# Kernel tuning notes

Measured on AMD Instinct MI355X. Metric: run time of the kernel, lower is better.

## Reference

```python
import jax, jax.numpy as jnp
import numpy as np

D_MODEL = 1024
N_HEADS = 16
D_HEAD = 64
B, S = 8, 1024
EPS = 1.1920929e-07  # torch.finfo(float32).eps, RMSNorm default eps=None


def setup_inputs() -> dict:
    key = jax.random.key(0)
    k1, k2, k3 = jax.random.split(key, 3)
    x = jax.random.normal(k1, (B, S, D_MODEL), dtype=jnp.float32)
    W_qkv = jax.random.normal(k2, (3 * N_HEADS * D_HEAD, D_MODEL), dtype=jnp.float32) * 0.02
    b_qkv = jnp.zeros((3 * N_HEADS * D_HEAD,), dtype=jnp.float32)
    W_o = jax.random.normal(k3, (D_MODEL, N_HEADS * D_HEAD), dtype=jnp.float32) * 0.02
    b_o = jnp.zeros((D_MODEL,), dtype=jnp.float32)
    return {"x": x, "W_qkv": W_qkv, "b_qkv": b_qkv, "W_o": W_o, "b_o": b_o}


def reference(x, W_qkv, b_qkv, W_o, b_o):
    # RMSNorm, no affine
    normed = x * jax.lax.rsqrt(jnp.mean(x * x, axis=-1, keepdims=True) + EPS)
    qkv = normed @ W_qkv.T + b_qkv                       # [b, s, 3*H*Dh]
    # packing order '(n_heads d_head n_qkv)' -> reshape (H, Dh, 3), unbind last
    qkv = qkv.reshape(*qkv.shape[:-1], N_HEADS, D_HEAD, 3)
    q, k, v = qkv[..., 0], qkv[..., 1], qkv[..., 2]       # [b, s, H, Dh]
    scores = jnp.einsum('bqhd,bkhd->bhqk', q, k)          # no 1/sqrt(d) scaling
    seq = x.shape[-2]
    causal_mask = jnp.triu(jnp.ones((seq, seq), dtype=bool), k=1)  # True above diag
    scores = jnp.where(causal_mask, -jnp.inf, scores)
    # NOTE: softmax over the QUERY axis (dim=-2), faithful to the source
    attn = jax.nn.softmax(scores, axis=-2)                # [b, h, q, k]
    z = jnp.einsum('bhqk,bkhd->bqhd', attn, v)            # [b, q, H, Dh]
    z = z.reshape(*z.shape[:-2], N_HEADS * D_HEAD)
    return z @ W_o.T + b_o
```

## Files before the change

### kernel.cpp

```cpp
#include <hip/hip_runtime.h>
#include <hip/hip_bf16.h>

typedef _Float16 f16;
typedef _Float16 f16x8 __attribute__((ext_vector_type(8)));
typedef _Float16 f16x4 __attribute__((ext_vector_type(4)));
typedef float f32x4 __attribute__((ext_vector_type(4)));

constexpr int Bb = 8, Ss = 1024, Hh = 16, DH = 64, DM = 1024, N3 = 3072;
constexpr int Mm = Bb * Ss;
constexpr float EPS = 1.1920929e-07f;

__device__ __forceinline__ void gll16(const f16* g, f16* l) {
    __builtin_amdgcn_global_load_lds(
        (__attribute__((address_space(1))) void*)(g),
        (__attribute__((address_space(3))) void*)(l), 16, 0, 0);
}

__global__ void prep_kernel(const float* __restrict__ x, f16* __restrict__ xh,
                            const float* __restrict__ Wqkv, const float* __restrict__ Wo,
                            f16* __restrict__ wq, f16* __restrict__ wo) {
    const int t = threadIdx.x;
    if (blockIdx.x < Mm) {
        const int row = blockIdx.x;
        float4 v = *(const float4*)(x + (size_t)row * DM + t * 4);
        float s = v.x * v.x + v.y * v.y + v.z * v.z + v.w * v.w;
#pragma unroll
        for (int o = 32; o > 0; o >>= 1) s += __shfl_down(s, o, 64);
        __shared__ float red[4];
        if ((t & 63) == 0) red[t >> 6] = s;
        __syncthreads();
        float tot = red[0] + red[1] + red[2] + red[3];
        float sc = rsqrtf(tot * (1.0f / DM) + EPS);
        f16x4 hv = {(f16)(v.x * sc), (f16)(v.y * sc), (f16)(v.z * sc), (f16)(v.w * sc)};
        *(f16x4*)(xh + (size_t)row * DM + t * 4) = hv;
    } else {
        int i = (blockIdx.x - Mm) * 256 + t;
        const int n1 = (N3 * DM) / 4;
        if (i < n1) {
            float4 v = ((const float4*)Wqkv)[i];
            f16x4 h = {(f16)v.x, (f16)v.y, (f16)v.z, (f16)v.w};
            ((f16x4*)wq)[i] = h;
        } else {
            int j = i - n1;
            float4 v = ((const float4*)Wo)[j];
            f16x4 h = {(f16)v.x, (f16)v.y, (f16)v.z, (f16)v.w};
            ((f16x4*)wo)[j] = h;
        }
    }
}

__launch_bounds__(256, 2)
__global__ void qkv_gemm(const f16* __restrict__ xh, const f16* __restrict__ wq,
                         const float* __restrict__ bqkv, f16* __restrict__ qk,
                         f16* __restrict__ vT) {
    __shared__ __align__(16) f16 As[128 * 64];
    __shared__ __align__(16) f16 Bs[128 * 64];
    const int t = threadIdx.x, lane = t & 63, w = t >> 6;
    const int bid = blockIdx.y * gridDim.x + blockIdx.x;
    const int swz = (bid & 7) * 192 + (bid >> 3);
    const int gm0 = (swz / 24) * 128, gn0 = (swz % 24) * 128;
    const int wm = (w >> 1) * 64, wn = (w & 1) * 64;
    const int srow = lane >> 3, sslot = (lane & 7) ^ srow;
    const int r15 = lane & 15, cs = lane >> 4;

    const f16* Ag = xh + (size_t)(gm0 + srow) * DM + sslot * 8;
    const f16* Bg = wq + (size_t)(gn0 + srow) * DM + sslot * 8;

    int aoff[4][2], boff[4][2];
#pragma unroll
    for (int i = 0; i < 4; ++i) {
        int Ra = wm + i * 16 + r15;
        aoff[i][0] = Ra * 64 + ((cs ^ (Ra & 7)) * 8);
        aoff[i][1] = Ra * 64 + (((cs + 4) ^ (Ra & 7)) * 8);
        int Rb = wn + i * 16 + r15;
        boff[i][0] = Rb * 64 + ((cs ^ (Rb & 7)) * 8);
        boff[i][1] = Rb * 64 + (((cs + 4) ^ (Rb & 7)) * 8);
    }
    f32x4 acc[4][4] = {};

    for (int k0 = 0; k0 < DM; k0 += 64) {
        __syncthreads();
#pragma unroll
        for (int j = 0; j < 4; ++j) {
            int c = w * 4 + j;
            gll16(Ag + (size_t)c * 8 * DM + k0, As + c * 512);
            gll16(Bg + (size_t)c * 8 * DM + k0, Bs + c * 512);
        }
        __syncthreads();
#pragma unroll
        for (int half = 0; half < 2; ++half) {
            f16x8 af[4], bf[4];
#pragma unroll
            for (int i = 0; i < 4; ++i) af[i] = *(const f16x8*)&As[aoff[i][half]];
#pragma unroll
            for (int i = 0; i < 4; ++i) bf[i] = *(const f16x8*)&Bs[boff[i][half]];
#pragma unroll
            for (int mi = 0; mi < 4; ++mi)
#pragma unroll
                for (int ni = 0; ni < 4; ++ni)
                    acc[mi][ni] = __builtin_amdgcn_mfma_f32_16x16x32_f16(af[mi], bf[ni], acc[mi][ni], 0, 0, 0);
        }
    }
#pragma unroll
    for (int mi = 0; mi < 4; ++mi) {
#pragma unroll
        for (int ni = 0; ni < 4; ++ni) {
            int jcol = gn0 + wn + ni * 16 + r15;
            float bb = bqkv[jcol];
            int h = jcol / 192, r = jcol % 192;
            int d = r / 3, which = r % 3;
            int m0 = gm0 + wm + mi * 16 + cs * 4;
            int b = m0 >> 10, s0 = m0 & 1023;
            int bh = b * Hh + h;
            if (which == 2) {
                f16x4 pv = {(f16)(acc[mi][ni][0] + bb), (f16)(acc[mi][ni][1] + bb),
                            (f16)(acc[mi][ni][2] + bb), (f16)(acc[mi][ni][3] + bb)};
                *(f16x4*)(vT + ((size_t)bh * DH + d) * Ss + s0) = pv;
            } else {
                size_t base = ((size_t)which * (Bb * Hh) + bh) * (size_t)(Ss * DH) + (size_t)s0 * DH + d;
#pragma unroll
                for (int jj = 0; jj < 4; ++jj)
                    qk[base + (size_t)jj * DH] = (f16)(acc[mi][ni][jj] + bb);
            }
        }
    }
}

__launch_bounds__(512, 2)
__global__ void colstats_kernel(const f16* __restrict__ qk, float* __restrict__ cbuf) {
    __shared__ __align__(16) f16 Qs[2][64 * 64];
    const int t = threadIdx.x, lane = t & 63, w = t >> 6;
    const int r15 = lane & 15, cs = lane >> 4;
    const int srow = lane >> 3, sslot = (lane & 7) ^ srow;
    const int bh = blockIdx.y, si = blockIdx.x;
    const int kA0 = si * 128, kB0 = (7 - si) * 128;
    const size_t hs = (size_t)(Bb * Hh) * (Ss * DH);
    const f16* qb = qk + (size_t)bh * (Ss * DH);
    const f16* kb = qb + hs;
    const int qt0 = 2 * si;

    const int kwA = kA0 + w * 16, kglobA = kwA + r15;
    const int kwB = kB0 + w * 16, kglobB = kwB + r15;
    f16x8 kfA0 = *(const f16x8*)(kb + (size_t)(kwA + r15) * DH + cs * 8);
    f16x8 kfA1 = *(const f16x8*)(kb + (size_t)(kwA + r15) * DH + 32 + cs * 8);
    f16x8 kfB0 = *(const f16x8*)(kb + (size_t)(kwB + r15) * DH + cs * 8);
    f16x8 kfB1 = *(const f16x8*)(kb + (size_t)(kwB + r15) * DH + 32 + cs * 8);

    gll16(qb + (size_t)(qt0 * 64 + w * 8 + srow) * DH + sslot * 8, Qs[0] + w * 512);
    __syncthreads();
    float la = 0.0f, lb = 0.0f;
    int cur = 0;

    for (int qt = qt0; qt < 16; ++qt) {
        if (qt + 1 < 16)
            gll16(qb + (size_t)((qt + 1) * 64 + w * 8 + srow) * DH + sslot * 8,
                  Qs[cur ^ 1] + w * 512);
        const bool engA = (qt * 64 + 63 >= kwA);
        const bool engB = (qt * 64 + 63 >= kwB);
        if (engA || engB) {
#pragma unroll
            for (int qs = 0; qs < 4; ++qs) {
                const int qb16 = qt * 64 + qs * 16;
                const bool nA = engA && (qb16 + 15 >= kwA);
                const bool nB = engB && (qb16 + 15 >= kwB);
                if (!(nA || nB)) continue;
                int Ra = qs * 16 + r15;
                f16x8 a0 = *(const f16x8*)&Qs[cur][Ra * 64 + ((cs ^ (Ra & 7)) * 8)];
                f16x8 a1 = *(const f16x8*)&Qs[cur][Ra * 64 + (((cs + 4) ^ (Ra & 7)) * 8)];
                if (nA) {
                    f32x4 sf = {};
                    sf = __builtin_amdgcn_mfma_f32_16x16x32_f16(a0, kfA0, sf, 0, 0, 0);
                    sf = __builtin_amdgcn_mfma_f32_16x16x32_f16(a1, kfA1, sf, 0, 0, 0);
#pragma unroll
                    for (int j = 0; j < 4; ++j) {
                        int q = qb16 + cs * 4 + j;
                        la += (q >= kglobA) ? __expf(sf[j]) : 0.0f;
                    }
                }
                if (nB) {
                    f32x4 sf = {};
                    sf = __builtin_amdgcn_mfma_f32_16x16x32_f16(a0, kfB0, sf, 0, 0, 0);
                    sf = __builtin_amdgcn_mfma_f32_16x16x32_f16(a1, kfB1, sf, 0, 0, 0);
#pragma unroll
                    for (int j = 0; j < 4; ++j) {
                        int q = qb16 + cs * 4 + j;
                        lb += (q >= kglobB) ? __expf(sf[j]) : 0.0f;
                    }
                }
            }
        }
        __syncthreads();
        cur ^= 1;
    }
    la += __shfl_xor(la, 16, 64);
    la += __shfl_xor(la, 32, 64);
    lb += __shfl_xor(lb, 16, 64);
    lb += __shfl_xor(lb, 32, 64);
    if (cs == 0) {
        cbuf[bh * Ss + kglobA] = logf(la);
        cbuf[bh * Ss + kglobB] = logf(lb);
    }
}

__launch_bounds__(512, 2)
__global__ void attnz_kernel(const f16* __restrict__ qk, const f16* __restrict__ vT,
                             const float* __restrict__ cbuf, f16* __restrict__ z) {
    __shared__ __align__(16) f16 Ks[64 * 64];
    __shared__ __align__(16) f16 Vs[64 * 64];
    __shared__ __align__(16) float cb[1024];
    const int t = threadIdx.x, lane = t & 63, w = t >> 6;
    const int r15 = lane & 15, cs = lane >> 4;
    const int srow = lane >> 3, sslot = (lane & 7) ^ srow;
    const int bh = blockIdx.y, si = blockIdx.x;
    const int qtA = si, qtB = 7 - si;
    const size_t hs = (size_t)(Bb * Hh) * (Ss * DH);
    const f16* qb = qk + (size_t)bh * (Ss * DH);
    const f16* kb = qb + hs;
    const f16* vb = vT + (size_t)bh * (DH * Ss);

    const int qwA = qtA * 128 + w * 16, qA = qwA + r15;
    const int qwB = qtB * 128 + w * 16, qB = qwB + r15;
    f16x8 aqA0 = *(const f16x8*)(qb + (size_t)(qwA + r15) * DH + cs * 8);
    f16x8 aqA1 = *(const f16x8*)(qb + (size_t)(qwA + r15) * DH + 32 + cs * 8);
    f16x8 aqB0 = *(const f16x8*)(qb + (size_t)(qwB + r15) * DH + cs * 8);
    f16x8 aqB1 = *(const f16x8*)(qb + (size_t)(qwB + r15) * DH + 32 + cs * 8);

    gll16(kb + (size_t)(w * 8 + srow) * DH + sslot * 8, Ks + w * 512);
    gll16(vb + (size_t)(w * 8 + srow) * Ss + sslot * 8, Vs + w * 512);
    {
        float2 c2 = *(const float2*)(cbuf + bh * Ss + t * 2);
        *(float2*)&cb[t * 2] = c2;
    }
    __syncthreads();
    f32x4 accA[4] = {}, accB[4] = {};
    const int nktA = 2 * qtA + 2, nktB = 2 * qtB + 2;
    const int sAl = ((cs & 1) * 2) * 16 + r15;
    const int sBl = sAl + 16;
    const bool hi = (cs >> 1) != 0;

    for (int kt = 0; kt < nktB; ++kt) {
        if (kt) {
            __syncthreads();
            gll16(kb + (size_t)(kt * 64 + w * 8 + srow) * DH + sslot * 8, Ks + w * 512);
            gll16(vb + (size_t)(w * 8 + srow) * Ss + kt * 64 + sslot * 8, Vs + w * 512);
            __syncthreads();
        }
        const int kb0 = kt * 64;
        const bool doA = (kt < nktA) && (kb0 <= qwA + 15);
        const bool doB = (kb0 <= qwB + 15);
        if (!(doA || doB)) continue;

        unsigned pkA[4][2], pkB[4][2];
#pragma unroll
        for (int tl = 0; tl < 4; ++tl) {
            const int kbase = kb0 + tl * 16;
            const bool nA = doA && (kbase <= qwA + 15);
            const bool nB = doB && (kbase <= qwB + 15);
            pkA[tl][0] = 0u; pkA[tl][1] = 0u;
            pkB[tl][0] = 0u; pkB[tl][1] = 0u;
            if (!(nA || nB)) continue;
            int Rk2 = tl * 16 + r15;
            f16x8 kf0 = *(const f16x8*)&Ks[Rk2 * 64 + ((cs ^ (Rk2 & 7)) * 8)];
            f16x8 kf1 = *(const f16x8*)&Ks[Rk2 * 64 + (((cs + 4) ^ (Rk2 & 7)) * 8)];
            f32x4 cv = *(const f32x4*)&cb[kbase + cs * 4];
            if (nA) {
                f32x4 sf = {};
                sf = __builtin_amdgcn_mfma_f32_16x16x32_f16(kf0, aqA0, sf, 0, 0, 0);
                sf = __builtin_amdgcn_mfma_f32_16x16x32_f16(kf1, aqA1, sf, 0, 0, 0);
                f16 p[4];
#pragma unroll
                for (int j = 0; j < 4; ++j) {
                    int k = kbase + cs * 4 + j;
                    p[j] = (f16)((k <= qA) ? __expf(sf[j] - cv[j]) : 0.0f);
                }
                union { f16 h[2]; unsigned u; } u0, u1;
                u0.h[0] = p[0]; u0.h[1] = p[1];
                u1.h[0] = p[2]; u1.h[1] = p[3];
                pkA[tl][0] = u0.u; pkA[tl][1] = u1.u;
            }
            if (nB) {
                f32x4 sf = {};
                sf = __builtin_amdgcn_mfma_f32_16x16x32_f16(kf0, aqB0, sf, 0, 0, 0);
                sf = __builtin_amdgcn_mfma_f32_16x16x32_f16(kf1, aqB1, sf, 0, 0, 0);
                f16 p[4];
#pragma unroll
                for (int j = 0; j < 4; ++j) {
                    int k = kbase + cs * 4 + j;
                    p[j] = (f16)((k <= qB) ? __expf(sf[j] - cv[j]) : 0.0f);
                }
                union { f16 h[2]; unsigned u; } u0, u1;
                u0.h[0] = p[0]; u0.h[1] = p[1];
                u1.h[0] = p[2]; u1.h[1] = p[3];
                pkB[tl][0] = u0.u; pkB[tl][1] = u1.u;
            }
        }
        f16x8 bfA[2], bfB[2];
        bool uA[2], uB[2];
#pragma unroll
        for (int c = 0; c < 2; ++c) {
            uA[c] = doA && (kb0 + c * 32 <= qwA + 15);
            uB[c] = doB && (kb0 + c * 32 <= qwB + 15);
            if (uA[c]) {
                unsigned a0 = (unsigned)__shfl((int)pkA[2 * c][0], sAl, 64);
                unsigned a1 = (unsigned)__shfl((int)pkA[2 * c][1], sAl, 64);
                unsigned a2 = (unsigned)__shfl((int)pkA[2 * c][0], sBl, 64);
                unsigned a3 = (unsigned)__shfl((int)pkA[2 * c][1], sBl, 64);
                unsigned b0_ = (unsigned)__shfl((int)pkA[2 * c + 1][0], sAl, 64);
                unsigned b1_ = (unsigned)__shfl((int)pkA[2 * c + 1][1], sAl, 64);
                unsigned b2_ = (unsigned)__shfl((int)pkA[2 * c + 1][0], sBl, 64);
                unsigned b3_ = (unsigned)__shfl((int)pkA[2 * c + 1][1], sBl, 64);
                union { unsigned u[4]; f16x8 v; } bf;
                bf.u[0] = hi ? b0_ : a0;
                bf.u[1] = hi ? b1_ : a1;
                bf.u[2] = hi ? b2_ : a2;
                bf.u[3] = hi ? b3_ : a3;
                bfA[c] = bf.v;
            }
            if (uB[c]) {
                unsigned a0 = (unsigned)__shfl((int)pkB[2 * c][0], sAl, 64);
                unsigned a1 = (unsigned)__shfl((int)pkB[2 * c][1], sAl, 64);
                unsigned a2 = (unsigned)__shfl((int)pkB[2 * c][0], sBl, 64);
                unsigned a3 = (unsigned)__shfl((int)pkB[2 * c][1], sBl, 64);
                unsigned b0_ = (unsigned)__shfl((int)pkB[2 * c + 1][0], sAl, 64);
                unsigned b1_ = (unsigned)__shfl((int)pkB[2 * c + 1][1], sAl, 64);
                unsigned b2_ = (unsigned)__shfl((int)pkB[2 * c + 1][0], sBl, 64);
                unsigned b3_ = (unsigned)__shfl((int)pkB[2 * c + 1][1], sBl, 64);
                union { unsigned u[4]; f16x8 v; } bf;
                bf.u[0] = hi ? b0_ : a0;
                bf.u[1] = hi ? b1_ : a1;
                bf.u[2] = hi ? b2_ : a2;
                bf.u[3] = hi ? b3_ : a3;
                bfB[c] = bf.v;
            }
        }
#pragma unroll
        for (int dt = 0; dt < 4; ++dt) {
            int Rv = dt * 16 + r15;
            f16x8 v0 = *(const f16x8*)&Vs[Rv * 64 + ((cs ^ (Rv & 7)) * 8)];
            f16x8 v1 = *(const f16x8*)&Vs[Rv * 64 + (((4 + cs) ^ (Rv & 7)) * 8)];
            if (uA[0]) accA[dt] = __builtin_amdgcn_mfma_f32_16x16x32_f16(v0, bfA[0], accA[dt], 0, 0, 0);
            if (uA[1]) accA[dt] = __builtin_amdgcn_mfma_f32_16x16x32_f16(v1, bfA[1], accA[dt], 0, 0, 0);
            if (uB[0]) accB[dt] = __builtin_amdgcn_mfma_f32_16x16x32_f16(v0, bfB[0], accB[dt], 0, 0, 0);
            if (uB[1]) accB[dt] = __builtin_amdgcn_mfma_f32_16x16x32_f16(v1, bfB[1], accB[dt], 0, 0, 0);
        }
    }
    const int b = bh >> 4, h = bh & 15;
#pragma unroll
    for (int dt = 0; dt < 4; ++dt) {
        f16x4 zvA = {(f16)accA[dt][0], (f16)accA[dt][1], (f16)accA[dt][2], (f16)accA[dt][3]};
        *(f16x4*)(z + ((size_t)(b * Ss + qA)) * DM + h * DH + dt * 16 + cs * 4) = zvA;
        f16x4 zvB = {(f16)accB[dt][0], (f16)accB[dt][1], (f16)accB[dt][2], (f16)accB[dt][3]};
        *(f16x4*)(z + ((size_t)(b * Ss + qB)) * DM + h * DH + dt * 16 + cs * 4) = zvB;
    }
}

__launch_bounds__(256, 2)
__global__ void out_gemm(const f16* __restrict__ z, const f16* __restrict__ wo,
                         const float* __restrict__ bo, float* __restrict__ out) {
    __shared__ __align__(16) f16 As[128 * 64];
    __shared__ __align__(16) f16 Bs[128 * 64];
    const int t = threadIdx.x, lane = t & 63, w = t >> 6;
    const int bid = blockIdx.y * gridDim.x + blockIdx.x;
    const int swz = (bid & 7) * 64 + (bid >> 3);
    const int gm0 = (swz / 8) * 128, gn0 = (swz % 8) * 128;
    const int wm = (w >> 1) * 64, wn = (w & 1) * 64;
    const int srow = lane >> 3, sslot = (lane & 7) ^ srow;
    const int r15 = lane & 15, cs = lane >> 4;

    const f16* Ag = z + (size_t)(gm0 + srow) * DM + sslot * 8;
    const f16* Bg = wo + (size_t)(gn0 + srow) * DM + sslot * 8;

    int aoff[4][2], boff[4][2];
#pragma unroll
    for (int i = 0; i < 4; ++i) {
        int Ra = wm + i * 16 + r15;
        aoff[i][0] = Ra * 64 + ((cs ^ (Ra & 7)) * 8);
        aoff[i][1] = Ra * 64 + (((cs + 4) ^ (Ra & 7)) * 8);
        int Rb = wn + i * 16 + r15;
        boff[i][0] = Rb * 64 + ((cs ^ (Rb & 7)) * 8);
        boff[i][1] = Rb * 64 + (((cs + 4) ^ (Rb & 7)) * 8);
    }
    f32x4 acc[4][4] = {};

    for (int k0 = 0; k0 < DM; k0 += 64) {
        __syncthreads();
#pragma unroll
        for (int j = 0; j < 4; ++j) {
            int c = w * 4 + j;
            gll16(Ag + (size_t)c * 8 * DM + k0, As + c * 512);
            gll16(Bg + (size_t)c * 8 * DM + k0, Bs + c * 512);
        }
        __syncthreads();
#pragma unroll
        for (int half = 0; half < 2; ++half) {
            f16x8 af[4], bf[4];
#pragma unroll
            for (int i = 0; i < 4; ++i) af[i] = *(const f16x8*)&As[aoff[i][half]];
#pragma unroll
            for (int i = 0; i < 4; ++i) bf[i] = *(const f16x8*)&Bs[boff[i][half]];
#pragma unroll
            for (int mi = 0; mi < 4; ++mi)
#pragma unroll
                for (int ni = 0; ni < 4; ++ni)
                    acc[mi][ni] = __builtin_amdgcn_mfma_f32_16x16x32_f16(af[mi], bf[ni], acc[mi][ni], 0, 0, 0);
        }
    }
#pragma unroll
    for (int mi = 0; mi < 4; ++mi) {
#pragma unroll
        for (int ni = 0; ni < 4; ++ni) {
            int n = gn0 + wn + ni * 16 + r15;
            float bb = bo[n];
#pragma unroll
            for (int jj = 0; jj < 4; ++jj) {
                int m = gm0 + wm + mi * 16 + cs * 4 + jj;
                out[(size_t)m * DM + n] = acc[mi][ni][jj] + bb;
            }
        }
    }
}

extern "C" void kernel_launch(void* const* d_in, const int* in_sizes, int n_in,
                              void* d_out, int out_size, void* d_ws, size_t ws_size,
                              hipStream_t stream) {
    (void)in_sizes; (void)n_in; (void)out_size; (void)ws_size;
    const float* x    = (const float*)d_in[0];
    const float* Wqkv = (const float*)d_in[1];
    const float* bqkv = (const float*)d_in[2];
    const float* Wo   = (const float*)d_in[3];
    const float* bo   = (const float*)d_in[4];
    float* out = (float*)d_out;

    char* ws = (char*)d_ws;
    f16* xh   = (f16*)ws;
    f16* z    = (f16*)ws;
    f16* wq   = (f16*)(ws + 16777216);
    f16* wo   = (f16*)(ws + 23068672);
    f16* qk   = (f16*)(ws + 25165824);
    f16* vT   = (f16*)(ws + 58720256);
    float* cbuf = (float*)(ws + 75497472);

    prep_kernel<<<Mm + 4096, 256, 0, stream>>>(x, xh, Wqkv, Wo, wq, wo);
    qkv_gemm<<<dim3(N3 / 128, Mm / 128), 256, 0, stream>>>(xh, wq, bqkv, qk, vT);
    colstats_kernel<<<dim3(4, Bb * Hh), 512, 0, stream>>>(qk, cbuf);
    attnz_kernel<<<dim3(4, Bb * Hh), 512, 0, stream>>>(qk, vT, cbuf, z);
    out_gemm<<<dim3(DM / 128, Mm / 128), 256, 0, stream>>>(z, wo, bo, out);
}
```

Before: 196.2 us.

## Permute QKV weight rows in prep and stage GEMM epilogue through LDS

The prep kernel now reorders W_qkv rows so that each 128-column output tile of the QKV GEMM holds only Q, only K or only V, with heads contiguous. The GEMM epilogue writes the accumulator tile into shared memory, padded to avoid bank conflicts, then stores it as 16-byte vectors: row-major for Q/K and transposed for V. This replaces scattered 2-byte stores, removing uncoalesced global writes at the cost of an extra LDS round trip and two barriers.

New measurement: 177.4 us. -9.6%, faster.

```diff
diff --git a/kernel.cpp b/kernel.cpp
--- a/kernel.cpp
+++ b/kernel.cpp
@@ -20,8 +20,9 @@
                             const float* __restrict__ Wqkv, const float* __restrict__ Wo,
                             f16* __restrict__ wq, f16* __restrict__ wo) {
     const int t = threadIdx.x;
-    if (blockIdx.x < Mm) {
-        const int row = blockIdx.x;
+    const int blk = blockIdx.x;
+    if (blk < Mm) {
+        const int row = blk;
         float4 v = *(const float4*)(x + (size_t)row * DM + t * 4);
         float s = v.x * v.x + v.y * v.y + v.z * v.z + v.w * v.w;
 #pragma unroll
@@ -33,19 +34,18 @@
         float sc = rsqrtf(tot * (1.0f / DM) + EPS);
         f16x4 hv = {(f16)(v.x * sc), (f16)(v.y * sc), (f16)(v.z * sc), (f16)(v.w * sc)};
         *(f16x4*)(xh + (size_t)row * DM + t * 4) = hv;
+    } else if (blk < Mm + N3) {
+        int j = blk - Mm;
+        int h = j / 192, r = j % 192, d = r / 3, wh = r % 3;
+        int rp = wh * 1024 + h * 64 + d;
+        float4 v = *(const float4*)(Wqkv + (size_t)j * DM + t * 4);
+        f16x4 hv = {(f16)v.x, (f16)v.y, (f16)v.z, (f16)v.w};
+        *(f16x4*)(wq + (size_t)rp * DM + t * 4) = hv;
     } else {
-        int i = (blockIdx.x - Mm) * 256 + t;
-        const int n1 = (N3 * DM) / 4;
-        if (i < n1) {
-            float4 v = ((const float4*)Wqkv)[i];
-            f16x4 h = {(f16)v.x, (f16)v.y, (f16)v.z, (f16)v.w};
-            ((f16x4*)wq)[i] = h;
-        } else {
-            int j = i - n1;
-            float4 v = ((const float4*)Wo)[j];
-            f16x4 h = {(f16)v.x, (f16)v.y, (f16)v.z, (f16)v.w};
-            ((f16x4*)wo)[j] = h;
-        }
+        int j = blk - Mm - N3;
+        float4 v = *(const float4*)(Wo + (size_t)j * DM + t * 4);
+        f16x4 hv = {(f16)v.x, (f16)v.y, (f16)v.z, (f16)v.w};
+        *(f16x4*)(wo + (size_t)j * DM + t * 4) = hv;
     }
 }
 
@@ -53,8 +53,10 @@
 __global__ void qkv_gemm(const f16* __restrict__ xh, const f16* __restrict__ wq,
                          const float* __restrict__ bqkv, f16* __restrict__ qk,
                          f16* __restrict__ vT) {
-    __shared__ __align__(16) f16 As[128 * 64];
-    __shared__ __align__(16) f16 Bs[128 * 64];
+    __shared__ __align__(16) f16 smem[17536];
+    f16* As = smem;
+    f16* Bs = smem + 8192;
+    f16* Cs = smem;
     const int t = threadIdx.x, lane = t & 63, w = t >> 6;
     const int bid = blockIdx.y * gridDim.x + blockIdx.x;
     const int swz = (bid & 7) * 192 + (bid >> 3);
@@ -101,27 +103,48 @@
                     acc[mi][ni] = __builtin_amdgcn_mfma_f32_16x16x32_f16(af[mi], bf[ni], acc[mi][ni], 0, 0, 0);
         }
     }
-#pragma unroll
-    for (int mi = 0; mi < 4; ++mi) {
-#pragma unroll
-        for (int ni = 0; ni < 4; ++ni) {
-            int jcol = gn0 + wn + ni * 16 + r15;
-            float bb = bqkv[jcol];
-            int h = jcol / 192, r = jcol % 192;
-            int d = r / 3, which = r % 3;
-            int m0 = gm0 + wm + mi * 16 + cs * 4;
-            int b = m0 >> 10, s0 = m0 & 1023;
-            int bh = b * Hh + h;
-            if (which == 2) {
-                f16x4 pv = {(f16)(acc[mi][ni][0] + bb), (f16)(acc[mi][ni][1] + bb),
-                            (f16)(acc[mi][ni][2] + bb), (f16)(acc[mi][ni][3] + bb)};
-                *(f16x4*)(vT + ((size_t)bh * DH + d) * Ss + s0) = pv;
-            } else {
-                size_t base = ((size_t)which * (Bb * Hh) + bh) * (size_t)(Ss * DH) + (size_t)s0 * DH + d;
-#pragma unroll
-                for (int jj = 0; jj < 4; ++jj)
-                    qk[base + (size_t)jj * DH] = (f16)(acc[mi][ni][jj] + bb);
-            }
+
+    const int which = gn0 >> 10;
+    const int CSTR = (which == 2) ? 137 : 136;
+    __syncthreads();
+#pragma unroll
+    for (int ni = 0; ni < 4; ++ni) {
+        int jcolp = gn0 + wn + ni * 16 + r15;
+        int rr = jcolp & 1023, hh = rr >> 6, dd = rr & 63;
+        float bb = bqkv[hh * 192 + dd * 3 + which];
+#pragma unroll
+        for (int mi = 0; mi < 4; ++mi)
+#pragma unroll
+            for (int jj = 0; jj < 4; ++jj)
+                Cs[(wm + mi * 16 + cs * 4 + jj) * CSTR + (wn + ni * 16 + r15)] =
+                    (f16)(acc[mi][ni][jj] + bb);
+    }
+    __syncthreads();
+    const int bglob = gm0 >> 10;
+    const int sbase = gm0 & 1023;
+    if (which < 2) {
+        f16* dstb = qk + (size_t)which * (Bb * Hh) * (Ss * DH);
+#pragma unroll
+        for (int it = 0; it < 8; ++it) {
+            int lin = it * 2048 + t * 8;
+            int row = lin >> 7, c0 = lin & 127;
+            f16x8 v = *(const f16x8*)&Cs[row * 136 + c0];
+            int rr = (gn0 + c0) & 1023;
+            int hh = rr >> 6, d0 = rr & 63;
+            *(f16x8*)(dstb + ((size_t)(bglob * Hh + hh)) * (Ss * DH) +
+                      (size_t)(sbase + row) * DH + d0) = v;
+        }
+    } else {
+#pragma unroll
+        for (int it = 0; it < 8; ++it) {
+            int col = it * 16 + (t >> 4);
+            int s0 = (t & 15) * 8;
+            f16x8 v;
+#pragma unroll
+            for (int e = 0; e < 8; ++e) v[e] = Cs[(s0 + e) * 137 + col];
+            int rr = (gn0 + col) & 1023;
+            int hh = rr >> 6, dd = rr & 63;
+            *(f16x8*)(vT + ((size_t)(bglob * Hh + hh) * DH + dd) * Ss + sbase + s0) = v;
         }
     }
 }
@@ -440,7 +463,7 @@
     f16* vT   = (f16*)(ws + 58720256);
     float* cbuf = (float*)(ws + 75497472);
 
-    prep_kernel<<<Mm + 4096, 256, 0, stream>>>(x, xh, Wqkv, Wo, wq, wo);
+    prep_kernel<<<Mm + N3 + DM, 256, 0, stream>>>(x, xh, Wqkv, Wo, wq, wo);
     qkv_gemm<<<dim3(N3 / 128, Mm / 128), 256, 0, stream>>>(xh, wq, bqkv, qk, vT);
     colstats_kernel<<<dim3(4, Bb * Hh), 512, 0, stream>>>(qk, cbuf);
     attnz_kernel<<<dim3(4, Bb * Hh), 512, 0, stream>>>(qk, vT, cbuf, z);
```
